# Kernel optimization log

Hardware: AMD Instinct MI355X
Metric: run time of the kernel (lower is better)

The kernel has to match this reference:

```python
import jax, jax.numpy as jnp
import numpy as np

N = 50000      # nodes
DEG = 16       # avg degree (random edges)
D = 128        # input_dim
H = 128        # hidden_dim
EPS = 1e-12


def setup_inputs() -> dict:
    key = jax.random.key(0)
    kx, ks, kd, kw1, kw2 = jax.random.split(key, 5)
    x = jax.random.normal(kx, (N, D), dtype=jnp.float32)
    src = jax.random.randint(ks, (N * DEG,), 0, N)
    dst = jax.random.randint(kd, (N * DEG,), 0, N)
    loops = jnp.arange(N)  # self-loops (AGNNConv default) -> every node has >=1 in-edge
    edge_index = jnp.stack([jnp.concatenate([src, loops]),
                            jnp.concatenate([dst, loops])]).astype(jnp.int64)
    W1 = jax.random.normal(kw1, (D, H), dtype=jnp.float32) / np.float32(np.sqrt(D))
    b1 = jnp.zeros((H,), dtype=jnp.float32)
    W2 = jax.random.normal(kw2, (H, H), dtype=jnp.float32) / np.float32(np.sqrt(H))
    b2 = jnp.zeros((H,), dtype=jnp.float32)
    beta1 = jnp.ones((), dtype=jnp.float32)
    beta2 = jnp.ones((), dtype=jnp.float32)
    return {"x": x, "edge_index": edge_index, "W1": W1, "b1": b1,
            "beta1": beta1, "W2": W2, "b2": b2, "beta2": beta2}


def _agnn_conv(x, edge_index, W, b, beta):
    n = x.shape[0]
    h = x @ W + b                                   # [N, H] linear projection
    # l2-normalize for cosine similarity
    hn = h * jax.lax.rsqrt(jnp.sum(h * h, axis=-1, keepdims=True) + EPS)
    src, dst = edge_index[0], edge_index[1]
    score = beta * jnp.sum(hn[src] * hn[dst], axis=-1)   # [E] beta * cos(h_i, h_j)
    # segment softmax over incoming edges of each destination node
    m = jax.ops.segment_max(score, dst, num_segments=n)
    e = jnp.exp(score - m[dst])
    denom = jax.ops.segment_sum(e, dst, num_segments=n)
    alpha = e / denom[dst]                               # [E]
    # weighted aggregation of source features
    return jax.ops.segment_sum(alpha[:, None] * h[src], dst, num_segments=n)


def reference(x, edge_index, W1, b1, beta1, W2, b2, beta2):
    h = jax.nn.relu(_agnn_conv(x, edge_index, W1, b1, beta1))
    # dropout (p=0.1) is identity in eval mode
    return jax.nn.relu(_agnn_conv(h, edge_index, W2, b2, beta2))
```

## Files before the change

kernel.cpp:

```cpp
#include <hip/hip_runtime.h>
#include <hip/hip_bf16.h>
#include <hip/hip_fp16.h>


#define FDIM 128
#define SCAN_CHUNK 2048
#define CONV_EPT 8
#define SCAT_EPT 4

__device__ __forceinline__ void convert_body(
    const void* __restrict__ ei, int E,
    int* __restrict__ src32, int* __restrict__ dst32,
    int* __restrict__ rank, int* __restrict__ counts, int cbid) {
  const int* eii = (const int*)ei;
  int lane = threadIdx.x & 63;
  int ok = (lane < 32) ? (eii[2 * lane + 1] == 0) : 1;
  bool is64 = (__ballot(ok) == ~0ull);

  int base = (cbid * 256 + threadIdx.x) * CONV_EPT;
  if (base + CONV_EPT <= E) {
    int s[CONV_EPT], d[CONV_EPT], r[CONV_EPT];
    if (is64) {
      const long long* p = (const long long*)ei;
      #pragma unroll
      for (int j = 0; j < CONV_EPT; ++j) { s[j] = (int)p[base + j]; d[j] = (int)p[E + base + j]; }
    } else {
      #pragma unroll
      for (int j = 0; j < CONV_EPT; ++j) { s[j] = eii[base + j]; d[j] = eii[E + base + j]; }
    }
    #pragma unroll
    for (int j = 0; j < CONV_EPT; ++j) r[j] = atomicAdd(&counts[d[j]], 1);
    #pragma unroll
    for (int j = 0; j < CONV_EPT; ++j) {
      src32[base + j] = s[j]; dst32[base + j] = d[j]; rank[base + j] = r[j];
    }
  } else {
    for (int j = 0; j < CONV_EPT; ++j) {
      int e = base + j; if (e >= E) break;
      int ss, dd;
      if (is64) { const long long* p = (const long long*)ei; ss = (int)p[e]; dd = (int)p[E + e]; }
      else      { ss = eii[e]; dd = eii[E + e]; }
      src32[e] = ss; dst32[e] = dd; rank[e] = atomicAdd(&counts[dd], 1);
    }
  }
}

template <typename TIN>
__device__ __forceinline__ void gemm32_body(
    const TIN* __restrict__ X, const float* __restrict__ Wg,
    const float* __restrict__ bias, __half* __restrict__ H16,
    float* __restrict__ rnorm, int N, int bid) {
  __shared__ float xt[128][36];
  int tid = threadIdx.x;
  int wv = tid >> 6, lane = tid & 63;
  int rowgrp = lane >> 5;
  int colgrp = lane & 31;
  int rbase = wv * 8 + rowgrp * 4;
  float4 bj = ((const float4*)bias)[colgrp];
  int r0 = bid * 32;

  for (int idx = tid; idx < 32 * 128; idx += 256) {
    int rr = idx >> 7, cc = idx & 127;
    int r = r0 + rr; if (r >= N) r = N - 1;
    xt[cc][rr] = (float)X[(size_t)r * 128 + cc];
  }
  __syncthreads();

  float4 a0 = bj, a1 = bj, a2 = bj, a3 = bj;
  #pragma unroll 8
  for (int k = 0; k < 128; ++k) {
    float4 w = *(const float4*)(Wg + k * 128 + 4 * colgrp);
    float4 xv = *(const float4*)&xt[k][rbase];
    a0.x += xv.x*w.x; a0.y += xv.x*w.y; a0.z += xv.x*w.z; a0.w += xv.x*w.w;
    a1.x += xv.y*w.x; a1.y += xv.y*w.y; a1.z += xv.y*w.z; a1.w += xv.y*w.w;
    a2.x += xv.z*w.x; a2.y += xv.z*w.y; a2.z += xv.z*w.z; a2.w += xv.z*w.w;
    a3.x += xv.w*w.x; a3.y += xv.w*w.y; a3.z += xv.w*w.z; a3.w += xv.w*w.w;
  }

  float4 av[4] = {a0, a1, a2, a3};
  #pragma unroll
  for (int rr = 0; rr < 4; ++rr) {
    float4 aa = av[rr];
    float s = aa.x*aa.x + aa.y*aa.y + aa.z*aa.z + aa.w*aa.w;
    #pragma unroll
    for (int m = 16; m; m >>= 1) s += __shfl_xor(s, m);
    int r = r0 + rbase + rr;
    if (r < N) {
      __half2 lo = __floats2half2_rn(aa.x, aa.y);
      __half2 hi = __floats2half2_rn(aa.z, aa.w);
      __half2* dst = (__half2*)(H16 + (size_t)r * 128 + 4 * colgrp);
      dst[0] = lo; dst[1] = hi;
      if (colgrp == 0) rnorm[r] = rsqrtf(s + 1e-12f);
    }
  }
}

__global__ __launch_bounds__(256) void gemm1_convert_kernel(
    const float* __restrict__ X, const float* __restrict__ Wg,
    const float* __restrict__ bias, __half* __restrict__ H16,
    float* __restrict__ rnorm, int N, int GB,
    const void* __restrict__ ei, int E,
    int* __restrict__ src32, int* __restrict__ dst32,
    int* __restrict__ rank, int* __restrict__ counts) {
  if ((int)blockIdx.x < GB)
    gemm32_body<float>(X, Wg, bias, H16, rnorm, N, blockIdx.x);
  else
    convert_body(ei, E, src32, dst32, rank, counts, blockIdx.x - GB);
}

__global__ __launch_bounds__(256) void scan_a_kernel(
    const int* __restrict__ counts, int* __restrict__ bsum, int N) {
  __shared__ int ws[4];
  int tid = threadIdx.x;
  int i0 = blockIdx.x * SCAN_CHUNK + tid * 8;
  int s = 0;
  if (i0 + 7 < N) {
    int4 a = *(const int4*)(counts + i0);
    int4 b = *(const int4*)(counts + i0 + 4);
    s = a.x + a.y + a.z + a.w + b.x + b.y + b.z + b.w;
  } else {
    #pragma unroll
    for (int j = 0; j < 8; ++j) if (i0 + j < N) s += counts[i0 + j];
  }
  #pragma unroll
  for (int m = 32; m; m >>= 1) s += __shfl_xor(s, m);
  int lane = tid & 63, wv = tid >> 6;
  if (lane == 0) ws[wv] = s;
  __syncthreads();
  if (tid == 0) bsum[blockIdx.x] = ws[0] + ws[1] + ws[2] + ws[3];
}

__global__ __launch_bounds__(256) void scan_c_kernel(
    const int* __restrict__ counts, const int* __restrict__ bsum,
    int* __restrict__ offsets, int N, int E) {
  __shared__ int wsum[4];
  int tid = threadIdx.x, lane = tid & 63, wv = tid >> 6;

  int bse = 0;
  for (int j = lane; j < (int)blockIdx.x; j += 64) bse += bsum[j];
  #pragma unroll
  for (int m = 32; m; m >>= 1) bse += __shfl_xor(bse, m);

  int i0 = blockIdx.x * SCAN_CHUNK + tid * 8;
  int v[8];
  if (i0 + 7 < N) {
    int4 a = *(const int4*)(counts + i0);
    int4 b = *(const int4*)(counts + i0 + 4);
    v[0]=a.x; v[1]=a.y; v[2]=a.z; v[3]=a.w;
    v[4]=b.x; v[5]=b.y; v[6]=b.z; v[7]=b.w;
  } else {
    #pragma unroll
    for (int j = 0; j < 8; ++j) v[j] = (i0 + j < N) ? counts[i0 + j] : 0;
  }
  int pre[8], t = 0;
  #pragma unroll
  for (int j = 0; j < 8; ++j) { pre[j] = t; t += v[j]; }
  int x = t;
  #pragma unroll
  for (int off = 1; off < 64; off <<= 1) {
    int u = __shfl_up(x, off);
    if (lane >= off) x += u;
  }
  if (lane == 63) wsum[wv] = x;
  __syncthreads();
  int waveoff = 0;
  #pragma unroll
  for (int w = 0; w < 4; ++w) if (w < wv) waveoff += wsum[w];
  int ebase = bse + waveoff + (x - t);
  #pragma unroll
  for (int j = 0; j < 8; ++j) {
    int i = i0 + j;
    if (i < N) offsets[i] = ebase + pre[j];
  }
  if (blockIdx.x == 0 && tid == 0) offsets[N] = E;
}

__global__ __launch_bounds__(256) void scatter_kernel(
    const int* __restrict__ src32, const int* __restrict__ dst32,
    const int* __restrict__ rank, const int* __restrict__ offsets, int E,
    int* __restrict__ csr_src) {
  int base = (blockIdx.x * 256 + threadIdx.x) * SCAT_EPT;
  if (base + SCAT_EPT <= E) {
    int4 s = *(const int4*)(src32 + base);
    int4 d = *(const int4*)(dst32 + base);
    int4 r = *(const int4*)(rank + base);
    int o0 = offsets[d.x], o1 = offsets[d.y], o2 = offsets[d.z], o3 = offsets[d.w];
    csr_src[o0 + r.x] = s.x;
    csr_src[o1 + r.y] = s.y;
    csr_src[o2 + r.z] = s.z;
    csr_src[o3 + r.w] = s.w;
  } else {
    for (int j = 0; j < SCAT_EPT; ++j) {
      int e = base + j; if (e >= E) break;
      csr_src[offsets[dst32[e]] + rank[e]] = src32[e];
    }
  }
}

template <typename TIN>
__global__ __launch_bounds__(256) void gemm_norm_kernel(
    const TIN* __restrict__ X, const float* __restrict__ Wg,
    const float* __restrict__ bias, __half* __restrict__ H16,
    float* __restrict__ rnorm, int N) {
  __shared__ float xt[128][72];
  int tid = threadIdx.x;
  int wv = tid >> 6, lane = tid & 63;
  int rowgrp = lane >> 5;
  int colgrp = lane & 31;
  int rbase = wv * 16 + rowgrp * 8;
  float4 bj = ((const float4*)bias)[colgrp];
  int r0 = blockIdx.x * 64;

  for (int idx = tid; idx < 64 * 128; idx += 256) {
    int rr = idx >> 7, cc = idx & 127;
    int r = r0 + rr; if (r >= N) r = N - 1;
    xt[cc][rr] = (float)X[(size_t)r * 128 + cc];
  }
  __syncthreads();

  float4 a[8];
  #pragma unroll
  for (int rr = 0; rr < 8; ++rr) a[rr] = bj;

  #pragma unroll 4
  for (int k = 0; k < 128; ++k) {
    float4 w = *(const float4*)(Wg + k * 128 + 4 * colgrp);
    float4 xv0 = *(const float4*)&xt[k][rbase];
    float4 xv1 = *(const float4*)&xt[k][rbase + 4];
    a[0].x += xv0.x*w.x; a[0].y += xv0.x*w.y; a[0].z += xv0.x*w.z; a[0].w += xv0.x*w.w;
    a[1].x += xv0.y*w.x; a[1].y += xv0.y*w.y; a[1].z += xv0.y*w.z; a[1].w += xv0.y*w.w;
    a[2].x += xv0.z*w.x; a[2].y += xv0.z*w.y; a[2].z += xv0.z*w.z; a[2].w += xv0.z*w.w;
    a[3].x += xv0.w*w.x; a[3].y += xv0.w*w.y; a[3].z += xv0.w*w.z; a[3].w += xv0.w*w.w;
    a[4].x += xv1.x*w.x; a[4].y += xv1.x*w.y; a[4].z += xv1.x*w.z; a[4].w += xv1.x*w.w;
    a[5].x += xv1.y*w.x; a[5].y += xv1.y*w.y; a[5].z += xv1.y*w.z; a[5].w += xv1.y*w.w;
    a[6].x += xv1.z*w.x; a[6].y += xv1.z*w.y; a[6].z += xv1.z*w.z; a[6].w += xv1.z*w.w;
    a[7].x += xv1.w*w.x; a[7].y += xv1.w*w.y; a[7].z += xv1.w*w.z; a[7].w += xv1.w*w.w;
  }

  #pragma unroll
  for (int rr = 0; rr < 8; ++rr) {
    float4 aa = a[rr];
    float s = aa.x*aa.x + aa.y*aa.y + aa.z*aa.z + aa.w*aa.w;
    #pragma unroll
    for (int m = 16; m; m >>= 1) s += __shfl_xor(s, m);
    int r = r0 + rbase + rr;
    if (r < N) {
      __half2 lo = __floats2half2_rn(aa.x, aa.y);
      __half2 hi = __floats2half2_rn(aa.z, aa.w);
      __half2* dst = (__half2*)(H16 + (size_t)r * 128 + 4 * colgrp);
      dst[0] = lo; dst[1] = hi;
      if (colgrp == 0) rnorm[r] = rsqrtf(s + 1e-12f);
    }
  }
}

template <bool OUT_HALF>
__global__ __launch_bounds__(256) void agg_kernel(
    const __half* __restrict__ H16, const float* __restrict__ rnorm,
    const float* __restrict__ beta_p, const int* __restrict__ offsets,
    const int* __restrict__ csr_src, void* __restrict__ Yp, int N) {
  int wid = (blockIdx.x * 256 + threadIdx.x) >> 6;
  int lane = threadIdx.x & 63;
  if (wid >= N) return;
  int g = lane >> 4;
  int l = lane & 15;
  const float4* H4 = (const float4*)H16;

  float4 hdv = H4[(size_t)wid * 16 + l];
  const __half2* hdp = (const __half2*)&hdv;
  float2 d0 = __half22float2(hdp[0]);
  float2 d1 = __half22float2(hdp[1]);
  float2 d2 = __half22float2(hdp[2]);
  float2 d3 = __half22float2(hdp[3]);
  float rdb = rnorm[wid] * beta_p[0];

  int e0 = offsets[wid], e1 = offsets[wid + 1];
  float denom = 0.f;
  float acc[8] = {0.f,0.f,0.f,0.f,0.f,0.f,0.f,0.f};

  int eA = e0 + g;
  bool vA = eA < e1;
  int sA = vA ? csr_src[eA] : wid;
  float4 hA = H4[(size_t)sA * 16 + l];
  float rA = rnorm[sA];

  int eB = eA + 4;
  bool vB = eB < e1;
  int sB = vB ? csr_src[eB] : wid;
  float4 hB = H4[(size_t)sB * 16 + l];
  float rB = rnorm[sB];

  for (int eb = e0; eb < e1; eb += 4) {
    int eC = eb + 8 + g;
    bool vC = eC < e1;
    int sC = vC ? csr_src[eC] : wid;
    float4 hC = H4[(size_t)sC * 16 + l];
    float rC = rnorm[sC];

    const __half2* hp = (const __half2*)&hA;
    float2 q0 = __half22float2(hp[0]);
    float2 q1 = __half22float2(hp[1]);
    float2 q2 = __half22float2(hp[2]);
    float2 q3 = __half22float2(hp[3]);
    float p = q0.x*d0.x + q0.y*d0.y + q1.x*d1.x + q1.y*d1.y
            + q2.x*d2.x + q2.y*d2.y + q3.x*d3.x + q3.y*d3.y;
    p += __shfl_xor(p, 1);
    p += __shfl_xor(p, 2);
    p += __shfl_xor(p, 4);
    p += __shfl_xor(p, 8);
    float w = vA ? __expf(p * rdb * rA) : 0.f;
    denom += w;
    acc[0] += w*q0.x; acc[1] += w*q0.y; acc[2] += w*q1.x; acc[3] += w*q1.y;
    acc[4] += w*q2.x; acc[5] += w*q2.y; acc[6] += w*q3.x; acc[7] += w*q3.y;

    vA = vB; hA = hB; rA = rB;
    vB = vC; hB = hC; rB = rC;
  }

  #pragma unroll
  for (int m = 16; m <= 32; m <<= 1) {
    denom += __shfl_xor(denom, m);
    #pragma unroll
    for (int j = 0; j < 8; ++j) acc[j] += __shfl_xor(acc[j], m);
  }
  if (g == 0) {
    float inv = 1.0f / denom;
    float o[8];
    #pragma unroll
    for (int j = 0; j < 8; ++j) o[j] = fmaxf(acc[j] * inv, 0.f);
    if constexpr (OUT_HALF) {
      float4 pack;
      __half2* hp2 = (__half2*)&pack;
      hp2[0] = __floats2half2_rn(o[0], o[1]);
      hp2[1] = __floats2half2_rn(o[2], o[3]);
      hp2[2] = __floats2half2_rn(o[4], o[5]);
      hp2[3] = __floats2half2_rn(o[6], o[7]);
      ((float4*)Yp)[(size_t)wid * 16 + l] = pack;
    } else {
      float4 o0 = {o[0], o[1], o[2], o[3]};
      float4 o1 = {o[4], o[5], o[6], o[7]};
      ((float4*)Yp)[(size_t)wid * 32 + 2 * l] = o0;
      ((float4*)Yp)[(size_t)wid * 32 + 2 * l + 1] = o1;
    }
  }
}

extern "C" void kernel_launch(void* const* d_in, const int* in_sizes, int n_in,
                              void* d_out, int out_size, void* d_ws, size_t ws_size,
                              hipStream_t stream) {
  const float* x     = (const float*)d_in[0];
  const void*  ei    = d_in[1];
  const float* W1    = (const float*)d_in[2];
  const float* b1    = (const float*)d_in[3];
  const float* beta1 = (const float*)d_in[4];
  const float* W2    = (const float*)d_in[5];
  const float* b2    = (const float*)d_in[6];
  const float* beta2 = (const float*)d_in[7];

  int N = in_sizes[0] / FDIM;
  int E = in_sizes[1] / 2;

  char* p = (char*)d_ws;
  auto alloc = [&](size_t bytes) {
    char* r = p; p += (bytes + 255) & ~size_t(255); return r;
  };
  int*    counts  = (int*)alloc(sizeof(int) * N);
  int*    offsets = (int*)alloc(sizeof(int) * (N + 1));
  int*    bsum    = (int*)alloc(sizeof(int) * 256);
  int*    src32   = (int*)alloc(sizeof(int) * E);
  int*    dst32   = (int*)alloc(sizeof(int) * E);
  int*    rank    = (int*)alloc(sizeof(int) * E);
  int*    csr     = (int*)alloc(sizeof(int) * E);
  __half* h16     = (__half*)alloc(sizeof(__half) * (size_t)N * FDIM);
  float*  rn      = (float*)alloc(sizeof(float) * N);
  __half* y1h     = (__half*)alloc(sizeof(__half) * (size_t)N * FDIM);

  hipMemsetAsync(counts, 0, sizeof(int) * N, stream);

  int gb1 = (N + 31) / 32;
  int cb  = (E + 256 * CONV_EPT - 1) / (256 * CONV_EPT);
  int sb  = (E + 256 * SCAT_EPT - 1) / (256 * SCAT_EPT);
  int nb  = (N + SCAN_CHUNK - 1) / SCAN_CHUNK;
  int gb2 = (N + 63) / 64;
  int ab  = (N + 3) / 4;

  gemm1_convert_kernel<<<gb1 + cb, 256, 0, stream>>>(
      x, W1, b1, h16, rn, N, gb1, ei, E, src32, dst32, rank, counts);
  scan_a_kernel<<<nb, 256, 0, stream>>>(counts, bsum, N);
  scan_c_kernel<<<nb, 256, 0, stream>>>(counts, bsum, offsets, N, E);
  scatter_kernel<<<sb, 256, 0, stream>>>(src32, dst32, rank, offsets, E, csr);

  agg_kernel<true><<<ab, 256, 0, stream>>>(h16, rn, beta1, offsets, csr, y1h, N);
  gemm_norm_kernel<__half><<<gb2, 256, 0, stream>>>(y1h, W2, b2, h16, rn, N);
  agg_kernel<false><<<ab, 256, 0, stream>>>(h16, rn, beta2, offsets, csr, d_out, N);
}
```

Before: 266.9 us.

## Use MFMA fp16 GEMMs with prepacked weights, reorder convert blocks, use fdot2 in aggregation

Replaces both scalar fp32 GEMM kernels with an MFMA 16x16x32 f16 path. The input is staged in LDS as fp16 and the weights are prepacked into fragment layout by a new small kernel. The edge-conversion part now handles 2 edges per thread with vector loads, and its blocks are scheduled before the GEMM blocks. The aggregation dot product uses the fdot2 builtin. Several independent changes land at once. Converting x and W1 to fp16 adds input rounding error, and the extra pack kernel adds a launch.

```diff
diff --git a/kernel.cpp b/kernel.cpp
--- a/kernel.cpp
+++ b/kernel.cpp
@@ -5,8 +5,97 @@
 
 #define FDIM 128
 #define SCAN_CHUNK 2048
-#define CONV_EPT 8
 #define SCAT_EPT 4
+
+typedef _Float16 f16x8 __attribute__((ext_vector_type(8)));
+typedef _Float16 f16x2 __attribute__((ext_vector_type(2)));
+typedef float f32x4 __attribute__((ext_vector_type(4)));
+
+#if defined(__has_builtin)
+#if __has_builtin(__builtin_amdgcn_fdot2)
+#define HAS_FDOT2 1
+#endif
+#endif
+
+__global__ __launch_bounds__(256) void pack_w_kernel(
+    const float* __restrict__ W1, const float* __restrict__ W2,
+    _Float16* __restrict__ wp1, _Float16* __restrict__ wp2) {
+  int t = blockIdx.x * 256 + threadIdx.x;
+  const float* W = (t < 2048) ? W1 : W2;
+  _Float16* wp   = (t < 2048) ? wp1 : wp2;
+  int tt = t & 2047;
+  int l = tt & 63, tile = tt >> 6, kt = tile & 3, nt = tile >> 2;
+  int kbase = kt * 32 + (l >> 4) * 8, col = nt * 16 + (l & 15);
+  f16x8 v;
+  #pragma unroll
+  for (int j = 0; j < 8; ++j) v[j] = (_Float16)W[(kbase + j) * 128 + col];
+  *(f16x8*)(wp + (size_t)tt * 8) = v;
+}
+
+template <typename TIN>
+__device__ __forceinline__ void mfma_gemm_body(
+    const TIN* __restrict__ X, const _Float16* __restrict__ wp,
+    const float* __restrict__ bias, __half* __restrict__ H16,
+    float* __restrict__ rnorm, int N, int bid) {
+  __shared__ _Float16 xt[64][136];
+  int tid = threadIdx.x;
+  int l = tid & 63, wv = tid >> 6;
+  int r0 = bid * 64;
+
+  for (int idx = tid; idx < 64 * 16; idx += 256) {
+    int row = idx >> 4, c8 = idx & 15;
+    int r = r0 + row; if (r >= N) r = N - 1;
+    f16x8 v;
+    if constexpr (sizeof(TIN) == 4) {
+      const float* px = (const float*)X + (size_t)r * 128 + c8 * 8;
+      float4 a = *(const float4*)px;
+      float4 b = *(const float4*)(px + 4);
+      v[0]=(_Float16)a.x; v[1]=(_Float16)a.y; v[2]=(_Float16)a.z; v[3]=(_Float16)a.w;
+      v[4]=(_Float16)b.x; v[5]=(_Float16)b.y; v[6]=(_Float16)b.z; v[7]=(_Float16)b.w;
+    } else {
+      v = *(const f16x8*)((const __half*)X + (size_t)r * 128 + c8 * 8);
+    }
+    *(f16x8*)&xt[row][c8 * 8] = v;
+  }
+  __syncthreads();
+
+  f32x4 acc[8];
+  #pragma unroll
+  for (int nt = 0; nt < 8; ++nt) acc[nt] = (f32x4){0.f, 0.f, 0.f, 0.f};
+
+  int arow = wv * 16 + (l & 15);
+  int koff = (l >> 4) * 8;
+  #pragma unroll
+  for (int kt = 0; kt < 4; ++kt) {
+    f16x8 afrag = *(const f16x8*)&xt[arow][kt * 32 + koff];
+    #pragma unroll
+    for (int nt = 0; nt < 8; ++nt) {
+      f16x8 bfrag = *(const f16x8*)(wp + (size_t)((nt * 4 + kt) * 64 + l) * 8);
+      acc[nt] = __builtin_amdgcn_mfma_f32_16x16x32_f16(afrag, bfrag, acc[nt], 0, 0, 0);
+    }
+  }
+
+  int col = l & 15, g = l >> 4;
+  float bv[8];
+  #pragma unroll
+  for (int nt = 0; nt < 8; ++nt) bv[nt] = bias[nt * 16 + col];
+
+  #pragma unroll
+  for (int j = 0; j < 4; ++j) {
+    float hv[8]; float s = 0.f;
+    #pragma unroll
+    for (int nt = 0; nt < 8; ++nt) { hv[nt] = acc[nt][j] + bv[nt]; s += hv[nt] * hv[nt]; }
+    s += __shfl_xor(s, 1); s += __shfl_xor(s, 2);
+    s += __shfl_xor(s, 4); s += __shfl_xor(s, 8);
+    int r = r0 + wv * 16 + g * 4 + j;
+    if (r < N) {
+      #pragma unroll
+      for (int nt = 0; nt < 8; ++nt)
+        H16[(size_t)r * 128 + nt * 16 + col] = __float2half(hv[nt]);
+      if (col == 0) rnorm[r] = rsqrtf(s + 1e-12f);
+    }
+  }
+}
 
 __device__ __forceinline__ void convert_body(
     const void* __restrict__ ei, int E,
@@ -17,26 +106,26 @@
   int ok = (lane < 32) ? (eii[2 * lane + 1] == 0) : 1;
   bool is64 = (__ballot(ok) == ~0ull);
 
-  int base = (cbid * 256 + threadIdx.x) * CONV_EPT;
-  if (base + CONV_EPT <= E) {
-    int s[CONV_EPT], d[CONV_EPT], r[CONV_EPT];
+  int base = (cbid * 256 + threadIdx.x) * 2;
+  if (base + 2 <= E) {
+    int s0, s1, d0, d1;
     if (is64) {
       const long long* p = (const long long*)ei;
-      #pragma unroll
-      for (int j = 0; j < CONV_EPT; ++j) { s[j] = (int)p[base + j]; d[j] = (int)p[E + base + j]; }
+      longlong2 sv = *(const longlong2*)(p + base);
+      longlong2 dv = *(const longlong2*)(p + E + base);
+      s0 = (int)sv.x; s1 = (int)sv.y; d0 = (int)dv.x; d1 = (int)dv.y;
     } else {
-      #pragma unroll
-      for (int j = 0; j < CONV_EPT; ++j) { s[j] = eii[base + j]; d[j] = eii[E + base + j]; }
-    }
-    #pragma unroll
-    for (int j = 0; j < CONV_EPT; ++j) r[j] = atomicAdd(&counts[d[j]], 1);
-    #pragma unroll
-    for (int j = 0; j < CONV_EPT; ++j) {
-      src32[base + j] = s[j]; dst32[base + j] = d[j]; rank[base + j] = r[j];
-    }
+      int2 sv = *(const int2*)(eii + base);
+      int2 dv = *(const int2*)(eii + E + base);
+      s0 = sv.x; s1 = sv.y; d0 = dv.x; d1 = dv.y;
+    }
+    int r0 = atomicAdd(&counts[d0], 1);
+    int r1 = atomicAdd(&counts[d1], 1);
+    *(int2*)(src32 + base) = make_int2(s0, s1);
+    *(int2*)(dst32 + base) = make_int2(d0, d1);
+    *(int2*)(rank + base)  = make_int2(r0, r1);
   } else {
-    for (int j = 0; j < CONV_EPT; ++j) {
-      int e = base + j; if (e >= E) break;
+    for (int e = base; e < E; ++e) {
       int ss, dd;
       if (is64) { const long long* p = (const long long*)ei; ss = (int)p[e]; dd = (int)p[E + e]; }
       else      { ss = eii[e]; dd = eii[E + e]; }
@@ -45,67 +134,24 @@
   }
 }
 
-template <typename TIN>
-__device__ __forceinline__ void gemm32_body(
-    const TIN* __restrict__ X, const float* __restrict__ Wg,
-    const float* __restrict__ bias, __half* __restrict__ H16,
-    float* __restrict__ rnorm, int N, int bid) {
-  __shared__ float xt[128][36];
-  int tid = threadIdx.x;
-  int wv = tid >> 6, lane = tid & 63;
-  int rowgrp = lane >> 5;
-  int colgrp = lane & 31;
-  int rbase = wv * 8 + rowgrp * 4;
-  float4 bj = ((const float4*)bias)[colgrp];
-  int r0 = bid * 32;
-
-  for (int idx = tid; idx < 32 * 128; idx += 256) {
-    int rr = idx >> 7, cc = idx & 127;
-    int r = r0 + rr; if (r >= N) r = N - 1;
-    xt[cc][rr] = (float)X[(size_t)r * 128 + cc];
-  }
-  __syncthreads();
-
-  float4 a0 = bj, a1 = bj, a2 = bj, a3 = bj;
-  #pragma unroll 8
-  for (int k = 0; k < 128; ++k) {
-    float4 w = *(const float4*)(Wg + k * 128 + 4 * colgrp);
-    float4 xv = *(const float4*)&xt[k][rbase];
-    a0.x += xv.x*w.x; a0.y += xv.x*w.y; a0.z += xv.x*w.z; a0.w += xv.x*w.w;
-    a1.x += xv.y*w.x; a1.y += xv.y*w.y; a1.z += xv.y*w.z; a1.w += xv.y*w.w;
-    a2.x += xv.z*w.x; a2.y += xv.z*w.y; a2.z += xv.z*w.z; a2.w += xv.z*w.w;
-    a3.x += xv.w*w.x; a3.y += xv.w*w.y; a3.z += xv.w*w.z; a3.w += xv.w*w.w;
-  }
-
-  float4 av[4] = {a0, a1, a2, a3};
-  #pragma unroll
-  for (int rr = 0; rr < 4; ++rr) {
-    float4 aa = av[rr];
-    float s = aa.x*aa.x + aa.y*aa.y + aa.z*aa.z + aa.w*aa.w;
-    #pragma unroll
-    for (int m = 16; m; m >>= 1) s += __shfl_xor(s, m);
-    int r = r0 + rbase + rr;
-    if (r < N) {
-      __half2 lo = __floats2half2_rn(aa.x, aa.y);
-      __half2 hi = __floats2half2_rn(aa.z, aa.w);
-      __half2* dst = (__half2*)(H16 + (size_t)r * 128 + 4 * colgrp);
-      dst[0] = lo; dst[1] = hi;
-      if (colgrp == 0) rnorm[r] = rsqrtf(s + 1e-12f);
-    }
-  }
-}
-
-__global__ __launch_bounds__(256) void gemm1_convert_kernel(
-    const float* __restrict__ X, const float* __restrict__ Wg,
-    const float* __restrict__ bias, __half* __restrict__ H16,
-    float* __restrict__ rnorm, int N, int GB,
+__global__ __launch_bounds__(256) void convert_gemm1_kernel(
     const void* __restrict__ ei, int E,
     int* __restrict__ src32, int* __restrict__ dst32,
-    int* __restrict__ rank, int* __restrict__ counts) {
-  if ((int)blockIdx.x < GB)
-    gemm32_body<float>(X, Wg, bias, H16, rnorm, N, blockIdx.x);
+    int* __restrict__ rank, int* __restrict__ counts, int CB,
+    const float* __restrict__ X, const _Float16* __restrict__ wp1,
+    const float* __restrict__ bias, __half* __restrict__ H16,
+    float* __restrict__ rnorm, int N) {
+  if ((int)blockIdx.x < CB)
+    convert_body(ei, E, src32, dst32, rank, counts, blockIdx.x);
   else
-    convert_body(ei, E, src32, dst32, rank, counts, blockIdx.x - GB);
+    mfma_gemm_body<float>(X, wp1, bias, H16, rnorm, N, blockIdx.x - CB);
+}
+
+__global__ __launch_bounds__(256) void gemm2_kernel(
+    const __half* __restrict__ X, const _Float16* __restrict__ wp,
+    const float* __restrict__ bias, __half* __restrict__ H16,
+    float* __restrict__ rnorm, int N) {
+  mfma_gemm_body<__half>(X, wp, bias, H16, rnorm, N, blockIdx.x);
 }
 
 __global__ __launch_bounds__(256) void scan_a_kernel(
@@ -197,63 +243,6 @@
   }
 }
 
-template <typename TIN>
-__global__ __launch_bounds__(256) void gemm_norm_kernel(
-    const TIN* __restrict__ X, const float* __restrict__ Wg,
-    const float* __restrict__ bias, __half* __restrict__ H16,
-    float* __restrict__ rnorm, int N) {
-  __shared__ float xt[128][72];
-  int tid = threadIdx.x;
-  int wv = tid >> 6, lane = tid & 63;
-  int rowgrp = lane >> 5;
-  int colgrp = lane & 31;
-  int rbase = wv * 16 + rowgrp * 8;
-  float4 bj = ((const float4*)bias)[colgrp];
-  int r0 = blockIdx.x * 64;
-
-  for (int idx = tid; idx < 64 * 128; idx += 256) {
-    int rr = idx >> 7, cc = idx & 127;
-    int r = r0 + rr; if (r >= N) r = N - 1;
-    xt[cc][rr] = (float)X[(size_t)r * 128 + cc];
-  }
-  __syncthreads();
-
-  float4 a[8];
-  #pragma unroll
-  for (int rr = 0; rr < 8; ++rr) a[rr] = bj;
-
-  #pragma unroll 4
-  for (int k = 0; k < 128; ++k) {
-    float4 w = *(const float4*)(Wg + k * 128 + 4 * colgrp);
-    float4 xv0 = *(const float4*)&xt[k][rbase];
-    float4 xv1 = *(const float4*)&xt[k][rbase + 4];
-    a[0].x += xv0.x*w.x; a[0].y += xv0.x*w.y; a[0].z += xv0.x*w.z; a[0].w += xv0.x*w.w;
-    a[1].x += xv0.y*w.x; a[1].y += xv0.y*w.y; a[1].z += xv0.y*w.z; a[1].w += xv0.y*w.w;
-    a[2].x += xv0.z*w.x; a[2].y += xv0.z*w.y; a[2].z += xv0.z*w.z; a[2].w += xv0.z*w.w;
-    a[3].x += xv0.w*w.x; a[3].y += xv0.w*w.y; a[3].z += xv0.w*w.z; a[3].w += xv0.w*w.w;
-    a[4].x += xv1.x*w.x; a[4].y += xv1.x*w.y; a[4].z += xv1.x*w.z; a[4].w += xv1.x*w.w;
-    a[5].x += xv1.y*w.x; a[5].y += xv1.y*w.y; a[5].z += xv1.y*w.z; a[5].w += xv1.y*w.w;
-    a[6].x += xv1.z*w.x; a[6].y += xv1.z*w.y; a[6].z += xv1.z*w.z; a[6].w += xv1.z*w.w;
-    a[7].x += xv1.w*w.x; a[7].y += xv1.w*w.y; a[7].z += xv1.w*w.z; a[7].w += xv1.w*w.w;
-  }
-
-  #pragma unroll
-  for (int rr = 0; rr < 8; ++rr) {
-    float4 aa = a[rr];
-    float s = aa.x*aa.x + aa.y*aa.y + aa.z*aa.z + aa.w*aa.w;
-    #pragma unroll
-    for (int m = 16; m; m >>= 1) s += __shfl_xor(s, m);
-    int r = r0 + rbase + rr;
-    if (r < N) {
-      __half2 lo = __floats2half2_rn(aa.x, aa.y);
-      __half2 hi = __floats2half2_rn(aa.z, aa.w);
-      __half2* dst = (__half2*)(H16 + (size_t)r * 128 + 4 * colgrp);
-      dst[0] = lo; dst[1] = hi;
-      if (colgrp == 0) rnorm[r] = rsqrtf(s + 1e-12f);
-    }
-  }
-}
-
 template <bool OUT_HALF>
 __global__ __launch_bounds__(256) void agg_kernel(
     const __half* __restrict__ H16, const float* __restrict__ rnorm,
@@ -302,8 +291,16 @@
     float2 q1 = __half22float2(hp[1]);
     float2 q2 = __half22float2(hp[2]);
     float2 q3 = __half22float2(hp[3]);
+#ifdef HAS_FDOT2
+    const f16x2* ha2 = (const f16x2*)&hA;
+    const f16x2* hd2 = (const f16x2*)&hdv;
+    float p = 0.f;
+    #pragma unroll
+    for (int t = 0; t < 4; ++t) p = __builtin_amdgcn_fdot2(ha2[t], hd2[t], p, false);
+#else
     float p = q0.x*d0.x + q0.y*d0.y + q1.x*d1.x + q1.y*d1.y
             + q2.x*d2.x + q2.y*d2.y + q3.x*d3.x + q3.y*d3.y;
+#endif
     p += __shfl_xor(p, 1);
     p += __shfl_xor(p, 2);
     p += __shfl_xor(p, 4);
@@ -364,33 +361,35 @@
   auto alloc = [&](size_t bytes) {
     char* r = p; p += (bytes + 255) & ~size_t(255); return r;
   };
-  int*    counts  = (int*)alloc(sizeof(int) * N);
-  int*    offsets = (int*)alloc(sizeof(int) * (N + 1));
-  int*    bsum    = (int*)alloc(sizeof(int) * 256);
-  int*    src32   = (int*)alloc(sizeof(int) * E);
-  int*    dst32   = (int*)alloc(sizeof(int) * E);
-  int*    rank    = (int*)alloc(sizeof(int) * E);
-  int*    csr     = (int*)alloc(sizeof(int) * E);
-  __half* h16     = (__half*)alloc(sizeof(__half) * (size_t)N * FDIM);
-  float*  rn      = (float*)alloc(sizeof(float) * N);
-  __half* y1h     = (__half*)alloc(sizeof(__half) * (size_t)N * FDIM);
+  int*      counts  = (int*)alloc(sizeof(int) * N);
+  int*      offsets = (int*)alloc(sizeof(int) * (N + 1));
+  int*      bsum    = (int*)alloc(sizeof(int) * 256);
+  int*      src32   = (int*)alloc(sizeof(int) * E);
+  int*      dst32   = (int*)alloc(sizeof(int) * E);
+  int*      rank    = (int*)alloc(sizeof(int) * E);
+  int*      csr     = (int*)alloc(sizeof(int) * E);
+  __half*   h16     = (__half*)alloc(sizeof(__half) * (size_t)N * FDIM);
+  float*    rn      = (float*)alloc(sizeof(float) * N);
+  __half*   y1h     = (__half*)alloc(sizeof(__half) * (size_t)N * FDIM);
+  _Float16* wp1     = (_Float16*)alloc(sizeof(_Float16) * 2048 * 8);
+  _Float16* wp2     = (_Float16*)alloc(sizeof(_Float16) * 2048 * 8);
 
   hipMemsetAsync(counts, 0, sizeof(int) * N, stream);
-
-  int gb1 = (N + 31) / 32;
-  int cb  = (E + 256 * CONV_EPT - 1) / (256 * CONV_EPT);
+  pack_w_kernel<<<16, 256, 0, stream>>>(W1, W2, wp1, wp2);
+
+  int cb  = (E + 511) / 512;
+  int gb  = (N + 63) / 64;
   int sb  = (E + 256 * SCAT_EPT - 1) / (256 * SCAT_EPT);
   int nb  = (N + SCAN_CHUNK - 1) / SCAN_CHUNK;
-  int gb2 = (N + 63) / 64;
   int ab  = (N + 3) / 4;
 
-  gemm1_convert_kernel<<<gb1 + cb, 256, 0, stream>>>(
-      x, W1, b1, h16, rn, N, gb1, ei, E, src32, dst32, rank, counts);
+  convert_gemm1_kernel<<<cb + gb, 256, 0, stream>>>(
+      ei, E, src32, dst32, rank, counts, cb, x, wp1, b1, h16, rn, N);
   scan_a_kernel<<<nb, 256, 0, stream>>>(counts, bsum, N);
   scan_c_kernel<<<nb, 256, 0, stream>>>(counts, bsum, offsets, N, E);
   scatter_kernel<<<sb, 256, 0, stream>>>(src32, dst32, rank, offsets, E, csr);
 
   agg_kernel<true><<<ab, 256, 0, stream>>>(h16, rn, beta1, offsets, csr, y1h, N);
-  gemm_norm_kernel<__half><<<gb2, 256, 0, stream>>>(y1h, W2, b2, h16, rn, N);
+  gemm2_kernel<<<gb, 256, 0, stream>>>(y1h, wp2, b2, h16, rn, N);
   agg_kernel<false><<<ab, 256, 0, stream>>>(h16, rn, beta2, offsets, csr, d_out, N);
 }
```

New measurement: 239.1 us. 1.12x faster.
